# Optimization experiments

Measured on AMD Instinct MI355X. Metric: run time of the kernel, lower is better.

## Reference

```python
import jax, jax.numpy as jnp
import numpy as np

B, N, E = 4, 2048, 16384
D, DM, NH, DH, FE = 10, 256, 8, 32, 9
K, KHOP, SIGMA = 30, 3, 1.5
_HOP_W = np.exp(-(np.arange(1, KHOP + 1) ** 2) / (2.0 * SIGMA ** 2))
_HOP_Z = float(_HOP_W.sum())


def _ln(x, g, b):
    mu = x.mean(-1, keepdims=True)
    var = ((x - mu) ** 2).mean(-1, keepdims=True)
    return g * (x - mu) * jax.lax.rsqrt(var + 1e-5) + b


def setup_inputs() -> dict:
    key = jax.random.key(0)
    ks = jax.random.split(key, 40)
    s = 0.02
    inp = {
        'bus_type': jax.random.randint(ks[0], (B, N), 0, 4, dtype=jnp.int32),
        'edge_index': jax.random.randint(ks[1], (B, 2, E), 0, N, dtype=jnp.int32),
        'G': 0.05 * jax.random.normal(ks[2], (B, N, N), jnp.float32),
        'Bm': 0.05 * jax.random.normal(ks[3], (B, N, N), jnp.float32),
        'P_set': jax.random.normal(ks[4], (B, N), jnp.float32),
        'Q_set': jax.random.normal(ks[5], (B, N), jnp.float32),
        'V0': jnp.stack([0.9 + 0.2 * jax.random.uniform(ks[6], (B, N)),
                         0.2 * jax.random.uniform(ks[7], (B, N)) - 0.1], -1).astype(jnp.float32),
        'edge_feat': jax.random.normal(ks[8], (B, E, FE), jnp.float32),
        'Win': s * jax.random.normal(ks[9], (2 * (4 + D), DM), jnp.float32),
        'b_in': jnp.zeros((DM,), jnp.float32),
        'Wq': s * jax.random.normal(ks[10], (DM, DM), jnp.float32),
        'bq': jnp.zeros((DM,), jnp.float32),
        'Wk': s * jax.random.normal(ks[11], (DM, DM), jnp.float32),
        'bk': jnp.zeros((DM,), jnp.float32),
        'Wv': s * jax.random.normal(ks[12], (DM, DM), jnp.float32),
        'bv': jnp.zeros((DM,), jnp.float32),
        'Wo': s * jax.random.normal(ks[13], (DM, DM), jnp.float32),
        'bo': jnp.zeros((DM,), jnp.float32),
        'We': s * jax.random.normal(ks[14], (FE, NH), jnp.float32),
        'be': jnp.zeros((NH,), jnp.float32),
        'ln1_g': jnp.ones((DM,), jnp.float32),
        'ln1_b': jnp.zeros((DM,), jnp.float32),
        'ln2_g': jnp.ones((DM,), jnp.float32),
        'ln2_b': jnp.zeros((DM,), jnp.float32),
        'Wf1': s * jax.random.normal(ks[15], (DM, 4 * DM), jnp.float32),
        'bf1': jnp.zeros((4 * DM,), jnp.float32),
        'Wf2': s * jax.random.normal(ks[16], (4 * DM, DM), jnp.float32),
        'bf2': jnp.zeros((DM,), jnp.float32),
        'Wth': s * jax.random.normal(ks[17], (K, DM, 1), jnp.float32),
        'bth': jnp.zeros((K, 1), jnp.float32),
        'Wvh': s * jax.random.normal(ks[18], (K, DM, 1), jnp.float32),
        'bvh': jnp.zeros((K, 1), jnp.float32),
        'Wm': s * jax.random.normal(ks[19], (K, DM, D), jnp.float32),
        'bm': jnp.zeros((K, D), jnp.float32),
    }
    return inp


def reference(bus_type, edge_index, G, Bm, P_set, Q_set, V0, edge_feat,
              Win, b_in, Wq, bq, Wk, bk, Wv, bv, Wo, bo, We, be,
              ln1_g, ln1_b, ln2_g, ln2_b, Wf1, bf1, Wf2, bf2,
              Wth, bth, Wvh, bvh, Wm, bm):
    slack = bus_type == 1
    pv = bus_type == 2
    p_maskf = (~slack).astype(G.dtype)            # theta updates / DP mask
    q_maskf = (~(slack | pv)).astype(G.dtype)     # v updates / DQ mask

    # electrical transition matrix T = rownorm(|Y| with zero diag), khop_source='yabs', khop_norm='row'
    A = jnp.sqrt(G * G + Bm * Bm) * (1.0 - jnp.eye(N, dtype=G.dtype))
    T = A / jnp.clip(A.sum(-1, keepdims=True), 1e-12, None)

    # flattened directed edges across batch for segment ops
    src = edge_index[:, 0, :]
    dst = edge_index[:, 1, :]
    offs = (jnp.arange(B, dtype=src.dtype) * N)[:, None]
    src_f = (src + offs).reshape(-1)
    dst_f = (dst + offs).reshape(-1)
    eb_f = (edge_feat @ We + be).reshape(-1, NH)  # per-edge per-head attention bias

    def khop(X):  # Gaussian-weighted K-hop diffusion: sum_h w_h T^h X / sum_h w_h
        Hh, acc = X, jnp.zeros_like(X)
        for hop in range(KHOP):
            Hh = jnp.einsum('bij,bjf->bif', T, Hh)
            acc = acc + float(_HOP_W[hop]) * Hh
        return acc / _HOP_Z

    def attn_block(x):  # edge-sparse multi-head self-attention + FFN
        q = (x @ Wq + bq).reshape(B * N, NH, DH)
        k = (x @ Wk + bk).reshape(B * N, NH, DH)
        vv = (x @ Wv + bv).reshape(B * N, NH, DH)
        score = (q[dst_f] * k[src_f]).sum(-1) / np.sqrt(DH) + eb_f  # [B*E, NH]
        mx = jax.ops.segment_max(score, dst_f, num_segments=B * N)
        p = jnp.exp(score - mx[dst_f])
        den = jax.ops.segment_sum(p, dst_f, num_segments=B * N)
        alpha = p / den[dst_f]
        agg = jax.ops.segment_sum(alpha[:, :, None] * vv[src_f], dst_f, num_segments=B * N)
        x = _ln(x + agg.reshape(B, N, DM) @ Wo + bo, ln1_g, ln1_b)
        h = jax.nn.relu(x @ Wf1 + bf1)
        return _ln(x + h @ Wf2 + bf2, ln2_g, ln2_b)

    def step(carry, hp):
        v, th, m = carry
        Wth_k, bth_k, Wvh_k, bvh_k, Wm_k, bm_k = hp
        e = v * jnp.cos(th)
        f = v * jnp.sin(th)
        Ire = jnp.einsum('bij,bj->bi', G, e) - jnp.einsum('bij,bj->bi', Bm, f)
        Iim = jnp.einsum('bij,bj->bi', G, f) + jnp.einsum('bij,bj->bi', Bm, e)
        DP = (P_set - (e * Ire + f * Iim)) * p_maskf
        DQ = (Q_set - (f * Ire - e * Iim)) * q_maskf
        ns = jnp.concatenate([jnp.stack([v, th, DP, DQ], -1), m], -1)  # [B,N,4+D]
        x = jnp.concatenate([ns, khop(ns)], -1) @ Win + b_in
        x = attn_block(x)
        dth = (x @ Wth_k + bth_k)[..., 0]
        dv = (x @ Wvh_k + bvh_k)[..., 0]
        m_new = x @ Wm_k + bm_k
        return (v + dv * q_maskf, th + dth * p_maskf, m_new), None

    v0, th0 = V0[..., 0], V0[..., 1]
    m0 = jnp.zeros((B, N, D), dtype=V0.dtype)
    (v, th, _), _ = jax.lax.scan(step, (v0, th0, m0), (Wth, bth, Wvh, bvh, Wm, bm))
    return jnp.stack([v, th], -1)
```

## Files before the change

kernel.cpp:

```cpp
#include <hip/hip_runtime.h>
#include <math.h>

typedef _Float16 f16x8 __attribute__((ext_vector_type(8)));
typedef _Float16 f16x4 __attribute__((ext_vector_type(4)));
typedef float f32x4 __attribute__((ext_vector_type(4)));

constexpr int B_ = 4, N_ = 2048, E_ = 16384;
constexpr int D_ = 10, DM_ = 256, NH_ = 8, FE_ = 9;
constexpr int BN_ = B_ * N_;
constexpr int BE_ = B_ * E_;

#define DEVI __device__ __forceinline__

DEVI _Float16 f2h(float f) { return (_Float16)f; }


__global__ void init_state(const int* __restrict__ bus, const float* __restrict__ V0,
                           float* v, float* th, float* m, float* pm, float* qm,
                           int* counts) {
  int t = blockIdx.x * blockDim.x + threadIdx.x;
  if (t >= BN_) return;
  int bt = bus[t];
  pm[t] = (bt == 1) ? 0.f : 1.f;
  qm[t] = (bt == 1 || bt == 2) ? 0.f : 1.f;
  v[t] = V0[2 * t];
  th[t] = V0[2 * t + 1];
  for (int d = 0; d < D_; ++d) m[(size_t)t * D_ + d] = 0.f;
  counts[t] = 0;
}

__global__ __launch_bounds__(256) void build_T_cast(const float* __restrict__ G,
    const float* __restrict__ Bm, _Float16* __restrict__ Tb,
    _Float16* __restrict__ Gh, _Float16* __restrict__ Bh) {
  int row = blockIdx.x;
  int i = row & (N_ - 1);
  const float* Gr = G + (size_t)row * N_;
  const float* Br = Bm + (size_t)row * N_;
  float a[8];
  float s = 0.f;
#pragma unroll
  for (int u = 0; u < 8; ++u) {
    int j = threadIdx.x + u * 256;
    float g = Gr[j], b = Br[j];
    if (Gh) { Gh[(size_t)row * N_ + j] = f2h(g); Bh[(size_t)row * N_ + j] = f2h(b); }
    float av = sqrtf(g * g + b * b);
    if (j == i) av = 0.f;
    a[u] = av;
    s += av;
  }
  __shared__ float red[4];
  for (int off = 32; off; off >>= 1) s += __shfl_down(s, off);
  int lane = threadIdx.x & 63, wave = threadIdx.x >> 6;
  if (lane == 0) red[wave] = s;
  __syncthreads();
  float tot = red[0] + red[1] + red[2] + red[3];
  float inv = 1.f / fmaxf(tot, 1e-12f);
#pragma unroll
  for (int u = 0; u < 8; ++u) {
    int j = threadIdx.x + u * 256;
    Tb[(size_t)row * N_ + j] = f2h(a[u] * inv);
  }
}

__global__ __launch_bounds__(256) void transpose16(const _Float16* __restrict__ in,
                                                   _Float16* __restrict__ out) {
  __shared__ float tile[64][65];
  int b = blockIdx.z;
  const _Float16* A = in + (size_t)b * N_ * N_;
  _Float16* O = out + (size_t)b * N_ * N_;
  int r0 = blockIdx.y * 64, c0 = blockIdx.x * 64;
  int tc = threadIdx.x & 63, tg = threadIdx.x >> 6;
#pragma unroll
  for (int i = 0; i < 16; ++i) {
    int r = tg * 16 + i;
    tile[r][tc] = (float)A[(size_t)(r0 + r) * N_ + c0 + tc];
  }
  __syncthreads();
#pragma unroll
  for (int i = 0; i < 16; ++i) {
    int r = tg * 16 + i;
    O[(size_t)(c0 + r) * N_ + r0 + tc] = f2h(tile[tc][r]);
  }
}

__global__ __launch_bounds__(256) void gemm_bat(const _Float16* __restrict__ A,
    const _Float16* __restrict__ Bt, _Float16* __restrict__ Cout,
    const _Float16* __restrict__ M1, const _Float16* __restrict__ M2,
    float w1, float w2, float w3) {
  int b = blockIdx.z;
  const _Float16* Ab = A + (size_t)b * N_ * N_;
  const _Float16* Bb = Bt + (size_t)b * N_ * N_;
  int wave = threadIdx.x >> 6, lane = threadIdx.x & 63;
  int wy = wave >> 1, wx = wave & 1;
  int m0 = blockIdx.x * 128 + wy * 64;
  int n0 = blockIdx.y * 128 + wx * 64;
  int lm = lane & 15, lq = lane >> 4;
  f32x4 acc[4][4] = {};
  const _Float16* Ap0 = Ab + (size_t)(m0 + lm) * N_ + lq * 8;
  const _Float16* Bp0 = Bb + (size_t)(n0 + lm) * N_ + lq * 8;
#pragma unroll 2
  for (int k = 0; k < N_; k += 32) {
    f16x8 af[4], bf[4];
#pragma unroll
    for (int i = 0; i < 4; ++i) {
      af[i] = *(const f16x8*)(Ap0 + (size_t)i * 16 * N_ + k);
      bf[i] = *(const f16x8*)(Bp0 + (size_t)i * 16 * N_ + k);
    }
#pragma unroll
    for (int mi = 0; mi < 4; ++mi)
#pragma unroll
      for (int ni = 0; ni < 4; ++ni)
        acc[mi][ni] = __builtin_amdgcn_mfma_f32_16x16x32_f16(af[mi], bf[ni],
                                                             acc[mi][ni], 0, 0, 0);
  }
  _Float16* Cb = Cout + (size_t)b * N_ * N_;
#pragma unroll
  for (int mi = 0; mi < 4; ++mi)
#pragma unroll
    for (int ni = 0; ni < 4; ++ni) {
      int col = n0 + ni * 16 + lm;
#pragma unroll
      for (int r = 0; r < 4; ++r) {
        int row = m0 + mi * 16 + lq * 4 + r;
        size_t o = (size_t)b * N_ * N_ + (size_t)row * N_ + col;
        float val = acc[mi][ni][r];
        if (M1) val = w3 * val + w1 * (float)M1[o] + w2 * (float)M2[o];
        Cb[(size_t)row * N_ + col] = f2h(val);
      }
    }
}

__global__ void edge_prep(const int* __restrict__ ei, const float* __restrict__ efeat,
    const float* __restrict__ We, const float* __restrict__ be,
    float* __restrict__ eb, int* __restrict__ srcf, int* __restrict__ dstf,
    int* __restrict__ counts) {
  int t = blockIdx.x * blockDim.x + threadIdx.x;
  if (t >= BE_) return;
  int b = t / E_, e = t - b * E_;
  int src = ei[(size_t)b * 2 * E_ + e];
  int dst = ei[(size_t)b * 2 * E_ + E_ + e];
  srcf[t] = src + b * N_;
  int df = dst + b * N_;
  dstf[t] = df;
  atomicAdd(&counts[df], 1);
  float fv[FE_];
#pragma unroll
  for (int f = 0; f < FE_; ++f) fv[f] = efeat[(size_t)t * FE_ + f];
#pragma unroll
  for (int h = 0; h < NH_; ++h) {
    float s = be[h];
#pragma unroll
    for (int f = 0; f < FE_; ++f) s += fv[f] * We[f * NH_ + h];
    eb[(size_t)t * NH_ + h] = s;
  }
}

__global__ void scan_kernel(const int* __restrict__ counts, int* __restrict__ offs,
                            int* __restrict__ cursor) {
  __shared__ int part[256];
  int t = threadIdx.x;
  int base = t * 32;
  int loc[32];
  int s = 0;
#pragma unroll
  for (int i = 0; i < 32; ++i) { loc[i] = counts[base + i]; s += loc[i]; }
  part[t] = s;
  __syncthreads();
  for (int off = 1; off < 256; off <<= 1) {
    int vv = (t >= off) ? part[t - off] : 0;
    __syncthreads();
    part[t] += vv;
    __syncthreads();
  }
  int run = part[t] - s;
#pragma unroll
  for (int i = 0; i < 32; ++i) {
    offs[base + i] = run;
    cursor[base + i] = run;
    run += loc[i];
  }
  if (t == 255) offs[BN_] = run;
}

__global__ void scatter_kernel(const int* __restrict__ dstf, int* cursor,
                               int* __restrict__ perm) {
  int t = blockIdx.x * blockDim.x + threadIdx.x;
  if (t >= BE_) return;
  int d = dstf[t];
  int pos = atomicAdd(&cursor[d], 1);
  perm[pos] = t;
}

__global__ void edge_reorder(const int* __restrict__ perm, const int* __restrict__ srcf,
                             const float* __restrict__ eb, int* __restrict__ sp,
                             float* __restrict__ ebp) {
  int j = blockIdx.x * 256 + threadIdx.x;
  if (j >= BE_) return;
  int e = perm[j];
  sp[j] = srcf[e];
#pragma unroll
  for (int h = 0; h < NH_; ++h) ebp[(size_t)j * 8 + h] = eb[(size_t)e * 8 + h];
}

__global__ void prep_weights(const float* Wq, const float* bq, const float* Wk,
    const float* bk, const float* Wv, const float* bvv, const float* Wo,
    const float* Wf1, const float* Wf2, const float* Wth, const float* bth,
    const float* Wvh, const float* bvh, const float* Wm, const float* bm,
    const float* Win,
    _Float16* Wqkvt, float* bqkv, _Float16* Wot,
    _Float16* Wf1t, _Float16* Wf2t, float* Wheads, float* bheads,
    _Float16* Wint) {
  int i = blockIdx.x * blockDim.x + threadIdx.x;
  if (i < 768 * 256) {
    int n = i >> 8, kk = i & 255;
    float val = n < 256 ? Wq[kk * 256 + n]
              : n < 512 ? Wk[kk * 256 + (n - 256)] : Wv[kk * 256 + (n - 512)];
    Wqkvt[n * 256 + kk] = f2h(val);
    return;
  }
  i -= 768 * 256;
  if (i < 256 * 256) {
    int n = i >> 8, kk = i & 255;
    Wot[n * 256 + kk] = f2h(Wo[kk * 256 + n]);
    return;
  }
  i -= 256 * 256;
  if (i < 1024 * 256) {
    int n = i >> 8, kk = i & 255;
    Wf1t[n * 256 + kk] = f2h(Wf1[kk * 1024 + n]);
    return;
  }
  i -= 1024 * 256;
  if (i < 256 * 1024) {
    int n = i >> 10, kk = i & 1023;
    Wf2t[n * 1024 + kk] = f2h(Wf2[kk * 256 + n]);
    return;
  }
  i -= 256 * 1024;
  if (i < 30 * 3072) {
    int k = i / 3072, j = i - k * 3072;
    int row = j / 12, o = j - row * 12;
    float val = o == 0 ? Wth[k * 256 + row]
              : o == 1 ? Wvh[k * 256 + row] : Wm[k * 2560 + row * 10 + (o - 2)];
    Wheads[k * 3072 + j] = val;
    return;
  }
  i -= 30 * 3072;
  if (i < 360) {
    int k = i / 12, o = i - k * 12;
    bheads[i] = o == 0 ? bth[k] : o == 1 ? bvh[k] : bm[k * 10 + (o - 2)];
    return;
  }
  i -= 360;
  if (i < 768) {
    bqkv[i] = i < 256 ? bq[i] : i < 512 ? bk[i - 256] : bvv[i - 512];
    return;
  }
  i -= 768;
  if (i < 256 * 32) {
    int n = i >> 5, kk = i & 31;
    Wint[n * 32 + kk] = (kk < 28) ? f2h(Win[kk * 256 + n]) : (_Float16)0.f;
  }
}


DEVI void ns_epilogue(int b, int row, float sre, float sim, int lane,
                      const float2* sef, const float* v, const float* th,
                      const float* P, const float* Q, const float* pm,
                      const float* qm, const float* m, _Float16* nsT) {
  for (int off = 1; off < 64; off <<= 1) {
    sre += __shfl_xor(sre, off);
    sim += __shfl_xor(sim, off);
  }
  if (lane < 16) {
    int node = b * N_ + row;
    float val;
    if (lane == 0) val = v[node];
    else if (lane == 1) val = th[node];
    else if (lane == 2) {
      float2 ef = sef[row];
      val = (P[node] - (ef.x * sre + ef.y * sim)) * pm[node];
    } else if (lane == 3) {
      float2 ef = sef[row];
      val = (Q[node] - (ef.y * sre - ef.x * sim)) * qm[node];
    } else if (lane < 14) val = m[(size_t)node * 10 + (lane - 4)];
    else val = 0.f;
    nsT[(size_t)b * 16 * N_ + (size_t)lane * N_ + row] = f2h(val);
  }
}

__global__ __launch_bounds__(256) void matvec_ns_f16(const _Float16* __restrict__ Gh,
    const _Float16* __restrict__ Bh, const float* __restrict__ v,
    const float* __restrict__ th, const float* __restrict__ P,
    const float* __restrict__ Q, const float* __restrict__ pm,
    const float* __restrict__ qm, const float* __restrict__ m,
    _Float16* __restrict__ nsT) {
  int b = blockIdx.y;
  __shared__ float2 sef[N_];
  for (int i = threadIdx.x; i < N_; i += 256) {
    float vv = v[b * N_ + i], tt = th[b * N_ + i];
    float sn, cs;
    __sincosf(tt, &sn, &cs);
    sef[i] = make_float2(vv * cs, vv * sn);
  }
  __syncthreads();
  int wave = threadIdx.x >> 6, lane = threadIdx.x & 63;
  for (int rr = 0; rr < 4; ++rr) {
    int row = blockIdx.x * 16 + wave * 4 + rr;
    const _Float16* Gr = Gh + ((size_t)b * N_ + row) * N_;
    const _Float16* Br = Bh + ((size_t)b * N_ + row) * N_;
    float sre = 0.f, sim = 0.f;
#pragma unroll
    for (int jj = 0; jj < 4; ++jj) {
      int j = lane * 8 + jj * 512;
      f16x8 g8 = *(const f16x8*)(Gr + j);
      f16x8 b8 = *(const f16x8*)(Br + j);
#pragma unroll
      for (int u = 0; u < 8; ++u) {
        float g = (float)g8[u], bb = (float)b8[u];
        float2 ef = sef[j + u];
        sre += g * ef.x - bb * ef.y;
        sim += g * ef.y + bb * ef.x;
      }
    }
    ns_epilogue(b, row, sre, sim, lane, sef, v, th, P, Q, pm, qm, m, nsT);
  }
}

__global__ __launch_bounds__(256) void matvec_ns_f32(const float* __restrict__ G,
    const float* __restrict__ Bm, const float* __restrict__ v,
    const float* __restrict__ th, const float* __restrict__ P,
    const float* __restrict__ Q, const float* __restrict__ pm,
    const float* __restrict__ qm, const float* __restrict__ m,
    _Float16* __restrict__ nsT) {
  int b = blockIdx.y;
  __shared__ float2 sef[N_];
  for (int i = threadIdx.x; i < N_; i += 256) {
    float vv = v[b * N_ + i], tt = th[b * N_ + i];
    float sn, cs;
    __sincosf(tt, &sn, &cs);
    sef[i] = make_float2(vv * cs, vv * sn);
  }
  __syncthreads();
  int wave = threadIdx.x >> 6, lane = threadIdx.x & 63;
  for (int rr = 0; rr < 4; ++rr) {
    int row = blockIdx.x * 16 + wave * 4 + rr;
    const float* Gr = G + ((size_t)b * N_ + row) * N_;
    const float* Br = Bm + ((size_t)b * N_ + row) * N_;
    float sre = 0.f, sim = 0.f;
#pragma unroll
    for (int jj = 0; jj < 8; ++jj) {
      int j = lane * 4 + jj * 256;
      float4 g4 = *(const float4*)(Gr + j);
      float4 b4 = *(const float4*)(Br + j);
      float2 e0 = sef[j], e1 = sef[j + 1], e2 = sef[j + 2], e3 = sef[j + 3];
      sre += g4.x * e0.x - b4.x * e0.y + g4.y * e1.x - b4.y * e1.y
           + g4.z * e2.x - b4.z * e2.y + g4.w * e3.x - b4.w * e3.y;
      sim += g4.x * e0.y + b4.x * e0.x + g4.y * e1.y + b4.y * e1.x
           + g4.z * e2.y + b4.z * e2.x + g4.w * e3.y + b4.w * e3.x;
    }
    ns_epilogue(b, row, sre, sim, lane, sef, v, th, P, Q, pm, qm, m, nsT);
  }
}

DEVI float khop_tile(const _Float16* __restrict__ Tm, const _Float16* __restrict__ Hin,
                     int b, int m0, int wave, int lm, int lq, int tid,
                     float (*red)[16][17]) {
  f32x4 acc = {0.f, 0.f, 0.f, 0.f};
  const _Float16* Trow = Tm + ((size_t)b * N_ + m0 + lm) * N_ + wave * 512 + lq * 8;
  const _Float16* Hrow = Hin + ((size_t)b * 16 + lm) * N_ + wave * 512 + lq * 8;
#pragma unroll 4
  for (int k = 0; k < 512; k += 32) {
    f16x8 a = *(const f16x8*)(Trow + k);
    f16x8 hb = *(const f16x8*)(Hrow + k);
    acc = __builtin_amdgcn_mfma_f32_16x16x32_f16(a, hb, acc, 0, 0, 0);
  }
#pragma unroll
  for (int r = 0; r < 4; ++r) red[wave][lq * 4 + r][lm] = acc[r];
  __syncthreads();
  int c = tid >> 4, rr = tid & 15;
  float s = red[0][rr][c] + red[1][rr][c] + red[2][rr][c] + red[3][rr][c];
  __syncthreads();
  return s;
}

__global__ __launch_bounds__(256) void khop_mix_input(
    const _Float16* __restrict__ Tmix, const _Float16* __restrict__ nsT,
    const _Float16* __restrict__ Wint, const float* __restrict__ bin,
    float* __restrict__ x0, _Float16* __restrict__ xh) {
  int b = blockIdx.y, m0 = blockIdx.x * 16;
  int tid = threadIdx.x;
  int wave = tid >> 6, lane = tid & 63;
  int lm = lane & 15, lq = lane >> 4;
  __shared__ float red[4][16][17];
  __shared__ _Float16 in28s[16][32];
  float s = khop_tile(Tmix, nsT, b, m0, wave, lm, lq, tid, red);
  int oc = tid >> 4, orr = tid & 15;
  size_t oidx = ((size_t)b * 16 + oc) * N_ + m0 + orr;
  if (oc < 14) {
    in28s[orr][oc] = nsT[oidx];
    in28s[orr][14 + oc] = f2h(s);
  } else if (oc == 14) {
    in28s[orr][28] = (_Float16)0.f;
    in28s[orr][29] = (_Float16)0.f;
  } else {
    in28s[orr][30] = (_Float16)0.f;
    in28s[orr][31] = (_Float16)0.f;
  }
  __syncthreads();
  f16x8 afrag = *(const f16x8*)(&in28s[lm][lq * 8]);
#pragma unroll
  for (int nt = 0; nt < 4; ++nt) {
    int n0 = wave * 64 + nt * 16;
    f16x8 bfrag = *(const f16x8*)(Wint + (size_t)(n0 + lm) * 32 + lq * 8);
    f32x4 c4 = {0.f, 0.f, 0.f, 0.f};
    c4 = __builtin_amdgcn_mfma_f32_16x16x32_f16(afrag, bfrag, c4, 0, 0, 0);
    float bv = bin[n0 + lm];
#pragma unroll
    for (int rg = 0; rg < 4; ++rg) {
      int rw = lq * 4 + rg;
      float val = c4[rg] + bv;
      size_t o = ((size_t)(b * N_ + m0 + rw)) * 256 + n0 + lm;
      x0[o] = val;
      xh[o] = f2h(val);
    }
  }
}

__global__ __launch_bounds__(256) void khop_kernel(const _Float16* __restrict__ Tb,
    const _Float16* __restrict__ HinT, _Float16* __restrict__ HoutT,
    float* __restrict__ accT, float w, int first) {
  int b = blockIdx.y, m0 = blockIdx.x * 16;
  int tid = threadIdx.x;
  int wave = tid >> 6, lane = tid & 63;
  int lm = lane & 15, lq = lane >> 4;
  __shared__ float red[4][16][17];
  float s = khop_tile(Tb, HinT, b, m0, wave, lm, lq, tid, red);
  int c = tid >> 4, r = tid & 15;
  size_t o = ((size_t)b * 16 + c) * N_ + m0 + r;
  if (HoutT) HoutT[o] = f2h(s);
  if (first) accT[o] = w * s; else accT[o] += w * s;
}

__global__ __launch_bounds__(256) void khop3_input(const _Float16* __restrict__ Tb,
    const _Float16* __restrict__ HinT, const _Float16* __restrict__ nsT,
    const float* __restrict__ accT, const _Float16* __restrict__ Wint,
    const float* __restrict__ bin, float hw2,
    float* __restrict__ x0, _Float16* __restrict__ xh) {
  int b = blockIdx.y, m0 = blockIdx.x * 16;
  int tid = threadIdx.x;
  int wave = tid >> 6, lane = tid & 63;
  int lm = lane & 15, lq = lane >> 4;
  __shared__ float red[4][16][17];
  __shared__ _Float16 in28s[16][32];
  float s = khop_tile(Tb, HinT, b, m0, wave, lm, lq, tid, red);
  int oc = tid >> 4, orr = tid & 15;
  size_t oidx = ((size_t)b * 16 + oc) * N_ + m0 + orr;
  if (oc < 14) {
    float atot = accT[oidx] + hw2 * s;
    in28s[orr][oc] = nsT[oidx];
    in28s[orr][14 + oc] = f2h(atot);
  } else if (oc == 14) {
    in28s[orr][28] = (_Float16)0.f;
    in28s[orr][29] = (_Float16)0.f;
  } else {
    in28s[orr][30] = (_Float16)0.f;
    in28s[orr][31] = (_Float16)0.f;
  }
  __syncthreads();
  f16x8 afrag = *(const f16x8*)(&in28s[lm][lq * 8]);
#pragma unroll
  for (int nt = 0; nt < 4; ++nt) {
    int n0 = wave * 64 + nt * 16;
    f16x8 bfrag = *(const f16x8*)(Wint + (size_t)(n0 + lm) * 32 + lq * 8);
    f32x4 c4 = {0.f, 0.f, 0.f, 0.f};
    c4 = __builtin_amdgcn_mfma_f32_16x16x32_f16(afrag, bfrag, c4, 0, 0, 0);
    float bv = bin[n0 + lm];
#pragma unroll
    for (int rg = 0; rg < 4; ++rg) {
      int rw = lq * 4 + rg;
      float val = c4[rg] + bv;
      size_t o = ((size_t)(b * N_ + m0 + rw)) * 256 + n0 + lm;
      x0[o] = val;
      xh[o] = f2h(val);
    }
  }
}

__global__ __launch_bounds__(256) void gemm_kernel(const _Float16* __restrict__ A,
    const _Float16* __restrict__ Wt, const float* __restrict__ bias,
    float* __restrict__ Cf, _Float16* __restrict__ Ch,
    int N, int K, int relu) {
  int wave = threadIdx.x >> 6, lane = threadIdx.x & 63;
  int wy = wave >> 1, wx = wave & 1;
  int m0 = blockIdx.x * 64 + wy * 32;
  int n0 = blockIdx.y * 64 + wx * 32;
  int lm = lane & 15, lq = lane >> 4;
  f32x4 acc[2][2] = {};
  const _Float16* A0 = A + (size_t)(m0 + lm) * K + lq * 8;
  const _Float16* A1 = A0 + (size_t)16 * K;
  const _Float16* B0 = Wt + (size_t)(n0 + lm) * K + lq * 8;
  const _Float16* B1 = B0 + (size_t)16 * K;
  for (int k = 0; k < K; k += 32) {
    f16x8 a0 = *(const f16x8*)(A0 + k);
    f16x8 a1 = *(const f16x8*)(A1 + k);
    f16x8 b0 = *(const f16x8*)(B0 + k);
    f16x8 b1 = *(const f16x8*)(B1 + k);
    acc[0][0] = __builtin_amdgcn_mfma_f32_16x16x32_f16(a0, b0, acc[0][0], 0, 0, 0);
    acc[0][1] = __builtin_amdgcn_mfma_f32_16x16x32_f16(a0, b1, acc[0][1], 0, 0, 0);
    acc[1][0] = __builtin_amdgcn_mfma_f32_16x16x32_f16(a1, b0, acc[1][0], 0, 0, 0);
    acc[1][1] = __builtin_amdgcn_mfma_f32_16x16x32_f16(a1, b1, acc[1][1], 0, 0, 0);
  }
#pragma unroll
  for (int tm = 0; tm < 2; ++tm)
#pragma unroll
    for (int tn = 0; tn < 2; ++tn) {
      int col = n0 + tn * 16 + lm;
      float bvv = bias ? bias[col] : 0.f;
#pragma unroll
      for (int r = 0; r < 4; ++r) {
        int row = m0 + tm * 16 + lq * 4 + r;
        float val = acc[tm][tn][r] + bvv;
        if (relu) val = fmaxf(val, 0.f);
        size_t o = (size_t)row * N + col;
        if (Cf) Cf[o] = val;
        if (Ch) Ch[o] = f2h(val);
      }
    }
}

__global__ __launch_bounds__(256) void attn_kernel(const _Float16* __restrict__ qkv,
    const int* __restrict__ offs, const int* __restrict__ sp,
    const float* __restrict__ ebp, _Float16* __restrict__ aggh) {
  int node = blockIdx.x * 4 + (threadIdx.x >> 6);
  int lane = threadIdx.x & 63;
  int h = lane >> 3;
  f16x4 qh = *(const f16x4*)(qkv + (size_t)node * 768 + lane * 4);
  float4 q4 = {(float)qh[0], (float)qh[1], (float)qh[2], (float)qh[3]};
  int beg = offs[node], end = offs[node + 1];
  float mx = -3.0e38f, den = 0.f;
  float4 acc = {0.f, 0.f, 0.f, 0.f};
  f16x4 kh_n = {}, vh_n = {};
  float eb_n = 0.f;
  if (beg < end) {
    int s = sp[beg];
    const _Float16* base = qkv + (size_t)s * 768 + lane * 4;
    kh_n = *(const f16x4*)(base + 256);
    vh_n = *(const f16x4*)(base + 512);
    eb_n = ebp[(size_t)beg * 8 + h];
  }
  for (int j = beg; j < end; ++j) {
    f16x4 kh = kh_n, vh = vh_n;
    float ebv = eb_n;
    if (j + 1 < end) {
      int s2 = sp[j + 1];
      const _Float16* b2 = qkv + (size_t)s2 * 768 + lane * 4;
      kh_n = *(const f16x4*)(b2 + 256);
      vh_n = *(const f16x4*)(b2 + 512);
      eb_n = ebp[(size_t)(j + 1) * 8 + h];
    }
    float p = q4.x * (float)kh[0] + q4.y * (float)kh[1]
            + q4.z * (float)kh[2] + q4.w * (float)kh[3];
    p += __shfl_xor(p, 1);
    p += __shfl_xor(p, 2);
    p += __shfl_xor(p, 4);
    float score = p * 0.17677669529663687f + ebv;
    float nm = fmaxf(mx, score);
    float sc = __expf(mx - nm);
    float w = __expf(score - nm);
    den = den * sc + w;
    acc.x = acc.x * sc + w * (float)vh[0];
    acc.y = acc.y * sc + w * (float)vh[1];
    acc.z = acc.z * sc + w * (float)vh[2];
    acc.w = acc.w * sc + w * (float)vh[3];
    mx = nm;
  }
  float inv = den > 0.f ? 1.f / den : 0.f;
  f16x4 o;
  o[0] = f2h(acc.x * inv);
  o[1] = f2h(acc.y * inv);
  o[2] = f2h(acc.z * inv);
  o[3] = f2h(acc.w * inv);
  *(f16x4*)(aggh + (size_t)node * DM_ + lane * 4) = o;
}

__global__ __launch_bounds__(256) void oproj_ln1(const _Float16* __restrict__ A,
    const _Float16* __restrict__ Wt, const float* __restrict__ bias,
    const float* __restrict__ res, const float* __restrict__ g,
    const float* __restrict__ bb, float* __restrict__ yF,
    _Float16* __restrict__ yH) {
  int m0 = blockIdx.x * 16;
  int wave = threadIdx.x >> 6, lane = threadIdx.x & 63;
  int lm = lane & 15, lq = lane >> 4;
  int n0 = wave * 64;
  f32x4 acc[4] = {};
  const _Float16* Ap = A + (size_t)(m0 + lm) * 256 + lq * 8;
  const _Float16* Bp = Wt + (size_t)(n0 + lm) * 256 + lq * 8;
  for (int k = 0; k < 256; k += 32) {
    f16x8 a0 = *(const f16x8*)(Ap + k);
#pragma unroll
    for (int nt = 0; nt < 4; ++nt) {
      f16x8 bf = *(const f16x8*)(Bp + nt * 16 * 256 + k);
      acc[nt] = __builtin_amdgcn_mfma_f32_16x16x32_f16(a0, bf, acc[nt], 0, 0, 0);
    }
  }
  float val[4][4];
  float rsum[4] = {}, rsq[4] = {};
#pragma unroll
  for (int nt = 0; nt < 4; ++nt) {
    int col = n0 + nt * 16 + lm;
    float bv = bias[col];
#pragma unroll
    for (int rg = 0; rg < 4; ++rg) {
      int row = m0 + lq * 4 + rg;
      float x = acc[nt][rg] + bv + res[(size_t)row * 256 + col];
      val[nt][rg] = x;
      rsum[rg] += x;
      rsq[rg] += x * x;
    }
  }
#pragma unroll
  for (int rg = 0; rg < 4; ++rg)
    for (int off = 1; off < 16; off <<= 1) {
      rsum[rg] += __shfl_xor(rsum[rg], off);
      rsq[rg] += __shfl_xor(rsq[rg], off);
    }
  __shared__ float redS[16][4], redQ[16][4];
  if (lm == 0) {
#pragma unroll
    for (int rg = 0; rg < 4; ++rg) {
      int r = lq * 4 + rg;
      redS[r][wave] = rsum[rg];
      redQ[r][wave] = rsq[rg];
    }
  }
  __syncthreads();
#pragma unroll
  for (int rg = 0; rg < 4; ++rg) {
    int r = lq * 4 + rg;
    float tS = redS[r][0] + redS[r][1] + redS[r][2] + redS[r][3];
    float tQ = redQ[r][0] + redQ[r][1] + redQ[r][2] + redQ[r][3];
    float mu = tS * (1.f / 256.f);
    float var = tQ * (1.f / 256.f) - mu * mu;
    float rs = rsqrtf(var + 1e-5f);
    int row = m0 + r;
#pragma unroll
    for (int nt = 0; nt < 4; ++nt) {
      int col = n0 + nt * 16 + lm;
      float y = g[col] * (val[nt][rg] - mu) * rs + bb[col];
      size_t o = (size_t)row * 256 + col;
      yF[o] = y;
      yH[o] = f2h(y);
    }
  }
}

struct FfnS2 {
  float xs[32][261];
  float whs[3072];
  float part[32][193];
};
union FfnU {
  _Float16 hs[32][1040];
  FfnS2 s2;
};

__global__ __launch_bounds__(512) void ffn_fused(const _Float16* __restrict__ A,
    const _Float16* __restrict__ Wf1t, const float* __restrict__ bf1,
    const _Float16* __restrict__ Wf2t, const float* __restrict__ bf2,
    const float* __restrict__ res, const float* __restrict__ g,
    const float* __restrict__ bb, const float* __restrict__ Wh,
    const float* __restrict__ bh, const float* __restrict__ pm,
    const float* __restrict__ qm, float* __restrict__ v,
    float* __restrict__ th, float* __restrict__ m) {
  constexpr int HP = 1040;
  int m0 = blockIdx.x * 32;
  int tid = threadIdx.x;
  int wave = tid >> 6, lane = tid & 63;
  int lm = lane & 15, lq = lane >> 4;
  __shared__ FfnU u;
  __shared__ float redS[32][8], redQ[32][8];
  {
    int n0 = wave * 128;
    f32x4 acc1[2][8] = {};
    const _Float16* Ap = A + (size_t)(m0 + lm) * 256 + lq * 8;
    const _Float16* Bp = Wf1t + (size_t)(n0 + lm) * 256 + lq * 8;
    for (int k = 0; k < 256; k += 32) {
      f16x8 a0 = *(const f16x8*)(Ap + k);
      f16x8 a1 = *(const f16x8*)(Ap + 16 * 256 + k);
#pragma unroll
      for (int nt = 0; nt < 8; ++nt) {
        f16x8 bf = *(const f16x8*)(Bp + nt * 16 * 256 + k);
        acc1[0][nt] = __builtin_amdgcn_mfma_f32_16x16x32_f16(a0, bf, acc1[0][nt], 0, 0, 0);
        acc1[1][nt] = __builtin_amdgcn_mfma_f32_16x16x32_f16(a1, bf, acc1[1][nt], 0, 0, 0);
      }
    }
#pragma unroll
    for (int mt = 0; mt < 2; ++mt)
#pragma unroll
      for (int nt = 0; nt < 8; ++nt) {
        int col = n0 + nt * 16 + lm;
        float bv = bf1[col];
#pragma unroll
        for (int rg = 0; rg < 4; ++rg) {
          int rloc = mt * 16 + lq * 4 + rg;
          u.hs[rloc][col] = f2h(fmaxf(acc1[mt][nt][rg] + bv, 0.f));
        }
      }
  }
  __syncthreads();
  float val[2][2][4];
  float rsum[2][4] = {}, rsq[2][4] = {};
  {
    int n0 = wave * 32;
    f32x4 acc2[2][2] = {};
    const _Float16* Bp = Wf2t + (size_t)(n0 + lm) * 1024 + lq * 8;
    for (int k = 0; k < 1024; k += 32) {
      f16x8 a0 = *(const f16x8*)(&u.hs[lm][k + lq * 8]);
      f16x8 a1 = *(const f16x8*)(&u.hs[16 + lm][k + lq * 8]);
      f16x8 b0 = *(const f16x8*)(Bp + k);
      f16x8 b1 = *(const f16x8*)(Bp + 16 * 1024 + k);
      acc2[0][0] = __builtin_amdgcn_mfma_f32_16x16x32_f16(a0, b0, acc2[0][0], 0, 0, 0);
      acc2[0][1] = __builtin_amdgcn_mfma_f32_16x16x32_f16(a0, b1, acc2[0][1], 0, 0, 0);
      acc2[1][0] = __builtin_amdgcn_mfma_f32_16x16x32_f16(a1, b0, acc2[1][0], 0, 0, 0);
      acc2[1][1] = __builtin_amdgcn_mfma_f32_16x16x32_f16(a1, b1, acc2[1][1], 0, 0, 0);
    }
#pragma unroll
    for (int mt = 0; mt < 2; ++mt)
#pragma unroll
      for (int nt = 0; nt < 2; ++nt) {
        int col = n0 + nt * 16 + lm;
        float bv = bf2[col];
#pragma unroll
        for (int rg = 0; rg < 4; ++rg) {
          int row = m0 + mt * 16 + lq * 4 + rg;
          float x = acc2[mt][nt][rg] + bv + res[(size_t)row * 256 + col];
          val[mt][nt][rg] = x;
          rsum[mt][rg] += x;
          rsq[mt][rg] += x * x;
        }
      }
  }
#pragma unroll
  for (int mt = 0; mt < 2; ++mt)
#pragma unroll
    for (int rg = 0; rg < 4; ++rg)
      for (int off = 1; off < 16; off <<= 1) {
        rsum[mt][rg] += __shfl_xor(rsum[mt][rg], off);
        rsq[mt][rg] += __shfl_xor(rsq[mt][rg], off);
      }
  if (lm == 0) {
#pragma unroll
    for (int mt = 0; mt < 2; ++mt)
#pragma unroll
      for (int rg = 0; rg < 4; ++rg) {
        int r = mt * 16 + lq * 4 + rg;
        redS[r][wave] = rsum[mt][rg];
        redQ[r][wave] = rsq[mt][rg];
      }
  }
  __syncthreads();
  for (int i = tid; i < 3072; i += 512) u.s2.whs[i] = Wh[i];
#pragma unroll
  for (int mt = 0; mt < 2; ++mt)
#pragma unroll
    for (int rg = 0; rg < 4; ++rg) {
      int r = mt * 16 + lq * 4 + rg;
      float tS = 0.f, tQ = 0.f;
#pragma unroll
      for (int w = 0; w < 8; ++w) { tS += redS[r][w]; tQ += redQ[r][w]; }
      float mu = tS * (1.f / 256.f);
      float var = tQ * (1.f / 256.f) - mu * mu;
      float rs = rsqrtf(var + 1e-5f);
#pragma unroll
      for (int nt = 0; nt < 2; ++nt) {
        int col = wave * 32 + nt * 16 + lm;
        u.s2.xs[r][col] = g[col] * (val[mt][nt][rg] - mu) * rs + bb[col];
      }
    }
  __syncthreads();
  {
    int rw = tid & 31, grp = tid >> 5;
    float pa[12] = {};
    for (int c = 0; c < 16; ++c) {
      int col = grp * 16 + c;
      float xv = u.s2.xs[rw][col];
#pragma unroll
      for (int o = 0; o < 12; ++o) pa[o] += xv * u.s2.whs[col * 12 + o];
    }
#pragma unroll
    for (int o = 0; o < 12; ++o) u.s2.part[rw][grp * 12 + o] = pa[o];
  }
  __syncthreads();
  if (tid < 32) {
    int node = m0 + tid;
    float tot[12];
#pragma unroll
    for (int o = 0; o < 12; ++o) {
      float s = bh[o];
#pragma unroll
      for (int grp = 0; grp < 16; ++grp) s += u.s2.part[tid][grp * 12 + o];
      tot[o] = s;
    }
    th[node] += tot[0] * pm[node];
    v[node] += tot[1] * qm[node];
#pragma unroll
    for (int d = 0; d < 10; ++d) m[(size_t)node * 10 + d] = tot[2 + d];
  }
}

__global__ void out_kernel(const float* __restrict__ v, const float* __restrict__ th,
                           float* __restrict__ out) {
  int t = blockIdx.x * blockDim.x + threadIdx.x;
  if (t >= BN_) return;
  out[2 * t] = v[t];
  out[2 * t + 1] = th[t];
}


extern "C" void kernel_launch(void* const* d_in, const int* in_sizes, int n_in,
                              void* d_out, int out_size, void* d_ws, size_t ws_size,
                              hipStream_t stream) {
  const int* bus = (const int*)d_in[0];
  const int* ei = (const int*)d_in[1];
  const float* G = (const float*)d_in[2];
  const float* Bm = (const float*)d_in[3];
  const float* P = (const float*)d_in[4];
  const float* Q = (const float*)d_in[5];
  const float* V0 = (const float*)d_in[6];
  const float* efeat = (const float*)d_in[7];
  const float* Win = (const float*)d_in[8];
  const float* bin = (const float*)d_in[9];
  const float* Wq = (const float*)d_in[10];
  const float* bq = (const float*)d_in[11];
  const float* Wk = (const float*)d_in[12];
  const float* bk = (const float*)d_in[13];
  const float* Wv = (const float*)d_in[14];
  const float* bv = (const float*)d_in[15];
  const float* Wo = (const float*)d_in[16];
  const float* bo = (const float*)d_in[17];
  const float* We = (const float*)d_in[18];
  const float* be = (const float*)d_in[19];
  const float* g1 = (const float*)d_in[20];
  const float* b1 = (const float*)d_in[21];
  const float* g2 = (const float*)d_in[22];
  const float* b2 = (const float*)d_in[23];
  const float* Wf1 = (const float*)d_in[24];
  const float* bf1 = (const float*)d_in[25];
  const float* Wf2 = (const float*)d_in[26];
  const float* bf2 = (const float*)d_in[27];
  const float* Wth = (const float*)d_in[28];
  const float* bth = (const float*)d_in[29];
  const float* Wvh = (const float*)d_in[30];
  const float* bvh = (const float*)d_in[31];
  const float* Wm = (const float*)d_in[32];
  const float* bm = (const float*)d_in[33];
  float* out = (float*)d_out;

  char* p = (char*)d_ws;
  auto alloc = [&](size_t bytes) -> void* {
    void* r = (void*)p;
    p += (bytes + 255) & ~(size_t)255;
    return r;
  };
  _Float16* Tb = (_Float16*)alloc((size_t)BN_ * N_ * 2);
  _Float16* nsT = (_Float16*)alloc((size_t)B_ * 16 * N_ * 2);
  _Float16* H1 = (_Float16*)alloc((size_t)B_ * 16 * N_ * 2);
  _Float16* H2 = (_Float16*)alloc((size_t)B_ * 16 * N_ * 2);
  float* accT = (float*)alloc((size_t)B_ * 16 * N_ * 4);
  _Float16* qkvh = (_Float16*)alloc((size_t)BN_ * 768 * 2);
  float* x0 = (float*)alloc((size_t)BN_ * 256 * 4);
  float* x1 = (float*)alloc((size_t)BN_ * 256 * 4);
  _Float16* xhA = (_Float16*)alloc((size_t)BN_ * 256 * 2);
  _Float16* xhB = (_Float16*)alloc((size_t)BN_ * 256 * 2);
  float* eb = (float*)alloc((size_t)BE_ * 8 * 4);
  float* ebp = (float*)alloc((size_t)BE_ * 8 * 4);
  int* srcf = (int*)alloc((size_t)BE_ * 4);
  int* dstf = (int*)alloc((size_t)BE_ * 4);
  int* sp = (int*)alloc((size_t)BE_ * 4);
  int* counts = (int*)alloc((size_t)BN_ * 4);
  int* offs = (int*)alloc((size_t)(BN_ + 1) * 4);
  int* cursor = (int*)alloc((size_t)BN_ * 4);
  int* perm = (int*)alloc((size_t)BE_ * 4);
  _Float16* Wqkvt = (_Float16*)alloc(768 * 256 * 2);
  _Float16* Wot = (_Float16*)alloc(256 * 256 * 2);
  _Float16* Wf1t = (_Float16*)alloc(1024 * 256 * 2);
  _Float16* Wf2t = (_Float16*)alloc(256 * 1024 * 2);
  _Float16* Wint = (_Float16*)alloc(256 * 32 * 2);
  float* Wheads = (float*)alloc(30 * 3072 * 4);
  float* bheads = (float*)alloc(30 * 12 * 4);
  float* bqkv = (float*)alloc(768 * 4);
  float* v = (float*)alloc((size_t)BN_ * 4);
  float* th = (float*)alloc((size_t)BN_ * 4);
  float* pm = (float*)alloc((size_t)BN_ * 4);
  float* qm = (float*)alloc((size_t)BN_ * 4);
  float* m = (float*)alloc((size_t)BN_ * 10 * 4);

  size_t nn2 = (size_t)B_ * N_ * N_ * 2;
  size_t used = (size_t)(p - (char*)d_ws);
  bool tmix_ok = (used + 3 * (nn2 + 256) <= ws_size);
  _Float16 *Tt = nullptr, *T2 = nullptr, *Tmix = nullptr;
  if (tmix_ok) {
    Tt = (_Float16*)alloc(nn2);
    T2 = (_Float16*)alloc(nn2);
    Tmix = (_Float16*)alloc(nn2);
  }
  used = (size_t)(p - (char*)d_ws);
  bool f16gb = (used + 2 * (nn2 + 256) <= ws_size);
  _Float16 *Gh = nullptr, *Bh = nullptr;
  if (f16gb) {
    Gh = (_Float16*)alloc(nn2);
    Bh = (_Float16*)alloc(nn2);
  }

  double hwd[3], z = 0.0;
  for (int i = 0; i < 3; ++i) {
    hwd[i] = exp(-((double)(i + 1) * (i + 1)) / (2.0 * 1.5 * 1.5));
    z += hwd[i];
  }
  float hw0 = (float)(hwd[0] / z), hw1 = (float)(hwd[1] / z), hw2 = (float)(hwd[2] / z);

  init_state<<<32, 256, 0, stream>>>(bus, V0, v, th, m, pm, qm, counts);
  build_T_cast<<<8192, 256, 0, stream>>>(G, Bm, Tb, Gh, Bh);
  if (tmix_ok) {
    transpose16<<<dim3(32, 32, 4), 256, 0, stream>>>(Tb, Tt);
    gemm_bat<<<dim3(16, 16, 4), 256, 0, stream>>>(Tb, Tt, T2,
        (const _Float16*)nullptr, (const _Float16*)nullptr, 0.f, 0.f, 0.f);
    gemm_bat<<<dim3(16, 16, 4), 256, 0, stream>>>(T2, Tt, Tmix, Tb, T2,
                                                  hw0, hw1, hw2);
  }
  edge_prep<<<BE_ / 256, 256, 0, stream>>>(ei, efeat, We, be, eb, srcf, dstf, counts);
  scan_kernel<<<1, 256, 0, stream>>>(counts, offs, cursor);
  scatter_kernel<<<BE_ / 256, 256, 0, stream>>>(dstf, cursor, perm);
  edge_reorder<<<BE_ / 256, 256, 0, stream>>>(perm, srcf, eb, sp, ebp);
  prep_weights<<<(887912 + 255) / 256, 256, 0, stream>>>(
      Wq, bq, Wk, bk, Wv, bv, Wo, Wf1, Wf2, Wth, bth, Wvh, bvh, Wm, bm, Win,
      Wqkvt, bqkv, Wot, Wf1t, Wf2t, Wheads, bheads, Wint);

  for (int k = 0; k < 30; ++k) {
    if (f16gb)
      matvec_ns_f16<<<dim3(128, 4), 256, 0, stream>>>(Gh, Bh, v, th, P, Q, pm, qm,
                                                      m, nsT);
    else
      matvec_ns_f32<<<dim3(128, 4), 256, 0, stream>>>(G, Bm, v, th, P, Q, pm, qm,
                                                      m, nsT);
    if (tmix_ok) {
      khop_mix_input<<<dim3(128, 4), 256, 0, stream>>>(Tmix, nsT, Wint, bin,
                                                       x0, xhA);
    } else {
      khop_kernel<<<dim3(128, 4), 256, 0, stream>>>(Tb, nsT, H1, accT, hw0, 1);
      khop_kernel<<<dim3(128, 4), 256, 0, stream>>>(Tb, H1, H2, accT, hw1, 0);
      khop3_input<<<dim3(128, 4), 256, 0, stream>>>(Tb, H2, nsT, accT, Wint, bin,
                                                    hw2, x0, xhA);
    }
    gemm_kernel<<<dim3(128, 12), 256, 0, stream>>>(xhA, Wqkvt, bqkv, nullptr, qkvh,
                                                   768, 256, 0);
    attn_kernel<<<2048, 256, 0, stream>>>(qkvh, offs, sp, ebp, xhB);
    oproj_ln1<<<512, 256, 0, stream>>>(xhB, Wot, bo, x0, g1, b1, x1, xhA);
    ffn_fused<<<256, 512, 0, stream>>>(xhA, Wf1t, bf1, Wf2t, bf2, x1, g2, b2,
                                       Wheads + k * 3072, bheads + k * 12,
                                       pm, qm, v, th, m);
  }
  out_kernel<<<32, 256, 0, stream>>>(v, th, out);
}
```

Baseline: 4.618 ms.

## Stage GEMM tiles through LDS with register prefetch for batched and QKV GEMMs

New measurement: 3.852 ms. 1.2x faster.

```diff
diff --git a/kernel.cpp b/kernel.cpp
--- a/kernel.cpp
+++ b/kernel.cpp
@@ -83,49 +83,103 @@
   }
 }
 
-__global__ __launch_bounds__(256) void gemm_bat(const _Float16* __restrict__ A,
+DEVI void gemm_core(const _Float16* __restrict__ A, const _Float16* __restrict__ Bt,
+                    int lda, int ldb, int K, int m0, int n0, int tid,
+                    _Float16 (*As)[72], _Float16 (*Bs)[72], f32x4 (*acc)[4]) {
+  int wave = tid >> 6, lane = tid & 63;
+  int wy = wave >> 1, wx = wave & 1;
+  int lm = lane & 15, lq = lane >> 4;
+  int srow = tid >> 1, sh = (tid & 1) * 32;
+  const _Float16* Ag = A + (size_t)(m0 + srow) * lda + sh;
+  const _Float16* Bg = Bt + (size_t)(n0 + srow) * ldb + sh;
+  f16x8 a4[4], b4[4];
+#pragma unroll
+  for (int c = 0; c < 4; ++c) {
+    a4[c] = *(const f16x8*)(Ag + c * 8);
+    b4[c] = *(const f16x8*)(Bg + c * 8);
+  }
+  for (int kt = 0; kt < K; kt += 64) {
+    __syncthreads();
+#pragma unroll
+    for (int c = 0; c < 4; ++c) {
+      *(f16x8*)(&As[srow][sh + c * 8]) = a4[c];
+      *(f16x8*)(&Bs[srow][sh + c * 8]) = b4[c];
+    }
+    __syncthreads();
+    if (kt + 64 < K) {
+#pragma unroll
+      for (int c = 0; c < 4; ++c) {
+        a4[c] = *(const f16x8*)(Ag + kt + 64 + c * 8);
+        b4[c] = *(const f16x8*)(Bg + kt + 64 + c * 8);
+      }
+    }
+#pragma unroll
+    for (int s = 0; s < 2; ++s) {
+      f16x8 af[4], bf[4];
+#pragma unroll
+      for (int i = 0; i < 4; ++i) {
+        af[i] = *(const f16x8*)(&As[wy * 64 + i * 16 + lm][s * 32 + lq * 8]);
+        bf[i] = *(const f16x8*)(&Bs[wx * 64 + i * 16 + lm][s * 32 + lq * 8]);
+      }
+#pragma unroll
+      for (int mi = 0; mi < 4; ++mi)
+#pragma unroll
+        for (int ni = 0; ni < 4; ++ni)
+          acc[mi][ni] = __builtin_amdgcn_mfma_f32_16x16x32_f16(af[mi], bf[ni],
+                                                               acc[mi][ni], 0, 0, 0);
+    }
+  }
+}
+
+__global__ __launch_bounds__(256) void gemm_bat2(const _Float16* __restrict__ A,
     const _Float16* __restrict__ Bt, _Float16* __restrict__ Cout,
     const _Float16* __restrict__ M1, const _Float16* __restrict__ M2,
     float w1, float w2, float w3) {
+  __shared__ _Float16 As[128][72], Bs[128][72];
   int b = blockIdx.z;
-  const _Float16* Ab = A + (size_t)b * N_ * N_;
-  const _Float16* Bb = Bt + (size_t)b * N_ * N_;
+  size_t base = (size_t)b * N_ * N_;
+  int m0 = blockIdx.x * 128, n0 = blockIdx.y * 128;
+  f32x4 acc[4][4] = {};
+  gemm_core(A + base, Bt + base, N_, N_, N_, m0, n0, threadIdx.x, As, Bs, acc);
   int wave = threadIdx.x >> 6, lane = threadIdx.x & 63;
   int wy = wave >> 1, wx = wave & 1;
-  int m0 = blockIdx.x * 128 + wy * 64;
-  int n0 = blockIdx.y * 128 + wx * 64;
   int lm = lane & 15, lq = lane >> 4;
-  f32x4 acc[4][4] = {};
-  const _Float16* Ap0 = Ab + (size_t)(m0 + lm) * N_ + lq * 8;
-  const _Float16* Bp0 = Bb + (size_t)(n0 + lm) * N_ + lq * 8;
-#pragma unroll 2
-  for (int k = 0; k < N_; k += 32) {
-    f16x8 af[4], bf[4];
-#pragma unroll
-    for (int i = 0; i < 4; ++i) {
-      af[i] = *(const f16x8*)(Ap0 + (size_t)i * 16 * N_ + k);
-      bf[i] = *(const f16x8*)(Bp0 + (size_t)i * 16 * N_ + k);
-    }
-#pragma unroll
-    for (int mi = 0; mi < 4; ++mi)
-#pragma unroll
-      for (int ni = 0; ni < 4; ++ni)
-        acc[mi][ni] = __builtin_amdgcn_mfma_f32_16x16x32_f16(af[mi], bf[ni],
-                                                             acc[mi][ni], 0, 0, 0);
-  }
-  _Float16* Cb = Cout + (size_t)b * N_ * N_;
 #pragma unroll
   for (int mi = 0; mi < 4; ++mi)
 #pragma unroll
     for (int ni = 0; ni < 4; ++ni) {
-      int col = n0 + ni * 16 + lm;
+      int col = n0 + wx * 64 + ni * 16 + lm;
 #pragma unroll
       for (int r = 0; r < 4; ++r) {
-        int row = m0 + mi * 16 + lq * 4 + r;
-        size_t o = (size_t)b * N_ * N_ + (size_t)row * N_ + col;
+        int row = m0 + wy * 64 + mi * 16 + lq * 4 + r;
+        size_t o = base + (size_t)row * N_ + col;
         float val = acc[mi][ni][r];
         if (M1) val = w3 * val + w1 * (float)M1[o] + w2 * (float)M2[o];
-        Cb[(size_t)row * N_ + col] = f2h(val);
+        Cout[o] = f2h(val);
+      }
+    }
+}
+
+__global__ __launch_bounds__(256) void qkv_ldst(const _Float16* __restrict__ A,
+    const _Float16* __restrict__ Wt, const float* __restrict__ bias,
+    _Float16* __restrict__ C) {
+  __shared__ _Float16 As[128][72], Bs[128][72];
+  int m0 = blockIdx.x * 128, n0 = blockIdx.y * 128;
+  f32x4 acc[4][4] = {};
+  gemm_core(A, Wt, 256, 256, 256, m0, n0, threadIdx.x, As, Bs, acc);
+  int wave = threadIdx.x >> 6, lane = threadIdx.x & 63;
+  int wy = wave >> 1, wx = wave & 1;
+  int lm = lane & 15, lq = lane >> 4;
+#pragma unroll
+  for (int mi = 0; mi < 4; ++mi)
+#pragma unroll
+    for (int ni = 0; ni < 4; ++ni) {
+      int col = n0 + wx * 64 + ni * 16 + lm;
+      float bv = bias[col];
+#pragma unroll
+      for (int r = 0; r < 4; ++r) {
+        int row = m0 + wy * 64 + mi * 16 + lq * 4 + r;
+        C[(size_t)row * 768 + col] = f2h(acc[mi][ni][r] + bv);
       }
     }
 }
@@ -487,48 +541,6 @@
   }
 }
 
-__global__ __launch_bounds__(256) void gemm_kernel(const _Float16* __restrict__ A,
-    const _Float16* __restrict__ Wt, const float* __restrict__ bias,
-    float* __restrict__ Cf, _Float16* __restrict__ Ch,
-    int N, int K, int relu) {
-  int wave = threadIdx.x >> 6, lane = threadIdx.x & 63;
-  int wy = wave >> 1, wx = wave & 1;
-  int m0 = blockIdx.x * 64 + wy * 32;
-  int n0 = blockIdx.y * 64 + wx * 32;
-  int lm = lane & 15, lq = lane >> 4;
-  f32x4 acc[2][2] = {};
-  const _Float16* A0 = A + (size_t)(m0 + lm) * K + lq * 8;
-  const _Float16* A1 = A0 + (size_t)16 * K;
-  const _Float16* B0 = Wt + (size_t)(n0 + lm) * K + lq * 8;
-  const _Float16* B1 = B0 + (size_t)16 * K;
-  for (int k = 0; k < K; k += 32) {
-    f16x8 a0 = *(const f16x8*)(A0 + k);
-    f16x8 a1 = *(const f16x8*)(A1 + k);
-    f16x8 b0 = *(const f16x8*)(B0 + k);
-    f16x8 b1 = *(const f16x8*)(B1 + k);
-    acc[0][0] = __builtin_amdgcn_mfma_f32_16x16x32_f16(a0, b0, acc[0][0], 0, 0, 0);
-    acc[0][1] = __builtin_amdgcn_mfma_f32_16x16x32_f16(a0, b1, acc[0][1], 0, 0, 0);
-    acc[1][0] = __builtin_amdgcn_mfma_f32_16x16x32_f16(a1, b0, acc[1][0], 0, 0, 0);
-    acc[1][1] = __builtin_amdgcn_mfma_f32_16x16x32_f16(a1, b1, acc[1][1], 0, 0, 0);
-  }
-#pragma unroll
-  for (int tm = 0; tm < 2; ++tm)
-#pragma unroll
-    for (int tn = 0; tn < 2; ++tn) {
-      int col = n0 + tn * 16 + lm;
-      float bvv = bias ? bias[col] : 0.f;
-#pragma unroll
-      for (int r = 0; r < 4; ++r) {
-        int row = m0 + tm * 16 + lq * 4 + r;
-        float val = acc[tm][tn][r] + bvv;
-        if (relu) val = fmaxf(val, 0.f);
-        size_t o = (size_t)row * N + col;
-        if (Cf) Cf[o] = val;
-        if (Ch) Ch[o] = f2h(val);
-      }
-    }
-}
-
 __global__ __launch_bounds__(256) void attn_kernel(const _Float16* __restrict__ qkv,
     const int* __restrict__ offs, const int* __restrict__ sp,
     const float* __restrict__ ebp, _Float16* __restrict__ aggh) {
@@ -673,7 +685,6 @@
     const float* __restrict__ bh, const float* __restrict__ pm,
     const float* __restrict__ qm, float* __restrict__ v,
     float* __restrict__ th, float* __restrict__ m) {
-  constexpr int HP = 1040;
   int m0 = blockIdx.x * 32;
   int tid = threadIdx.x;
   int wave = tid >> 6, lane = tid & 63;
@@ -924,10 +935,10 @@
   build_T_cast<<<8192, 256, 0, stream>>>(G, Bm, Tb, Gh, Bh);
   if (tmix_ok) {
     transpose16<<<dim3(32, 32, 4), 256, 0, stream>>>(Tb, Tt);
-    gemm_bat<<<dim3(16, 16, 4), 256, 0, stream>>>(Tb, Tt, T2,
+    gemm_bat2<<<dim3(16, 16, 4), 256, 0, stream>>>(Tb, Tt, T2,
         (const _Float16*)nullptr, (const _Float16*)nullptr, 0.f, 0.f, 0.f);
-    gemm_bat<<<dim3(16, 16, 4), 256, 0, stream>>>(T2, Tt, Tmix, Tb, T2,
-                                                  hw0, hw1, hw2);
+    gemm_bat2<<<dim3(16, 16, 4), 256, 0, stream>>>(T2, Tt, Tmix, Tb, T2,
+                                                   hw0, hw1, hw2);
   }
   edge_prep<<<BE_ / 256, 256, 0, stream>>>(ei, efeat, We, be, eb, srcf, dstf, counts);
   scan_kernel<<<1, 256, 0, stream>>>(counts, offs, cursor);
@@ -953,8 +964,7 @@
       khop3_input<<<dim3(128, 4), 256, 0, stream>>>(Tb, H2, nsT, accT, Wint, bin,
                                                     hw2, x0, xhA);
     }
-    gemm_kernel<<<dim3(128, 12), 256, 0, stream>>>(xhA, Wqkvt, bqkv, nullptr, qkvh,
-                                                   768, 256, 0);
+    qkv_ldst<<<dim3(64, 6), 256, 0, stream>>>(xhA, Wqkvt, bqkv, qkvh);
     attn_kernel<<<2048, 256, 0, stream>>>(qkvh, offs, sp, ebp, xhB);
     oproj_ln1<<<512, 256, 0, stream>>>(xhB, Wot, bo, x0, g1, b1, x1, xhA);
     ffn_fused<<<256, 512, 0, stream>>>(xhA, Wf1t, bf1, Wf2t, bf2, x1, g2, b2,
```
